# Optimization experiments

Hardware: AMD Instinct MI355X
Metric: run time of the kernel (lower is better)

Reference implementation:

```python
import jax, jax.numpy as jnp
import numpy as np

NEG_SLOPE = 0.2  # PyG GATConv default leaky_relu slope


def gat_layer(x, src, dst, W, a_src, a_dst, bias, heads, d, concat):
    # x: [N, in_dim]; src/dst: [E] (edges flow src -> dst, self-loops included)
    N = x.shape[0]
    h = (x @ W).reshape(N, heads, d)                      # [N, H, D]
    alpha_src = jnp.einsum('nhd,hd->nh', h, a_src)        # [N, H]
    alpha_dst = jnp.einsum('nhd,hd->nh', h, a_dst)        # [N, H]
    e = jax.nn.leaky_relu(alpha_src[src] + alpha_dst[dst], NEG_SLOPE)  # [E, H]
    # softmax over incoming edges of each destination node (segment softmax)
    m = jax.ops.segment_max(e, dst, num_segments=N)       # [N, H]
    ex = jnp.exp(e - m[dst])
    s = jax.ops.segment_sum(ex, dst, num_segments=N)      # [N, H]
    alpha = ex / s[dst]                                   # [E, H]
    msg = h[src] * alpha[..., None]                       # [E, H, D]
    out = jax.ops.segment_sum(msg, dst, num_segments=N)   # [N, H, D]
    out = out.reshape(N, heads * d) if concat else out.mean(axis=1)
    return out + bias


def setup_inputs() -> dict:
    key = jax.random.key(0)
    ks = jax.random.split(key, 12)
    N, E = 10000, 320000
    in_dim, hidden, heads, out_dim = 256, 64, 4, 40
    x = jax.random.normal(ks[0], (N, in_dim), dtype=jnp.float32)
    edge_index = jax.random.randint(ks[1], (2, E), 0, N, dtype=jnp.int64)
    s = 0.1
    return {
        'x': x,
        'edge_index': edge_index,
        'W1': jax.random.normal(ks[2], (in_dim, heads * hidden), jnp.float32) * s,
        'att_src1': jax.random.normal(ks[3], (heads, hidden), jnp.float32) * s,
        'att_dst1': jax.random.normal(ks[4], (heads, hidden), jnp.float32) * s,
        'bias1': jnp.zeros((heads * hidden,), jnp.float32),
        'W2': jax.random.normal(ks[5], (heads * hidden, out_dim), jnp.float32) * s,
        'att_src2': jax.random.normal(ks[6], (1, out_dim), jnp.float32) * s,
        'att_dst2': jax.random.normal(ks[7], (1, out_dim), jnp.float32) * s,
        'bias2': jnp.zeros((out_dim,), jnp.float32),
    }


def reference(x, edge_index, W1, att_src1, att_dst1, bias1, W2, att_src2, att_dst2, bias2):
    N = x.shape[0]
    # PyG GATConv adds self-loops by default
    loop = jnp.arange(N, dtype=edge_index.dtype)
    src = jnp.concatenate([edge_index[0], loop])
    dst = jnp.concatenate([edge_index[1], loop])
    h = gat_layer(x, src, dst, W1, att_src1, att_dst1, bias1, heads=4, d=64, concat=True)
    h = jax.nn.relu(h)
    out = gat_layer(h, src, dst, W2, att_src2, att_dst2, bias2, heads=1, d=40, concat=False)
    return jax.nn.log_softmax(out, axis=1)
```

## Files before the change

### kernel.cpp

```cpp
#include <hip/hip_runtime.h>
#include <hip/hip_bf16.h>
#include <math.h>

#define IN_DIM 256
#define C1 256
#define H1 4
#define OUT_DIM 40
#define W2PAD 48
#define NEG_SLOPE 0.2f
#define DSTRIDE 128

typedef __attribute__((ext_vector_type(8))) short bf16x8;
typedef __attribute__((ext_vector_type(4))) float f32x4;
typedef __attribute__((ext_vector_type(2))) float f32x2;

#define XS_LD 264

__device__ __forceinline__ unsigned short f2bf(float f) {
    union { float f; unsigned u; } c; c.f = f;
    unsigned r = c.u + 0x7fffu + ((c.u >> 16) & 1u);
    return (unsigned short)(r >> 16);
}

__device__ __forceinline__ unsigned char f2fp8(float f) {
    return (unsigned char)__builtin_amdgcn_cvt_pk_fp8_f32(f, 0.f, 0, false);
}

__device__ __forceinline__ float sel4(float4 v, int h) {
    float r = v.x;
    r = (h == 1) ? v.y : r;
    r = (h == 2) ? v.z : r;
    r = (h == 3) ? v.w : r;
    return r;
}

__device__ __forceinline__ float leaky(float v) {
    return (v >= 0.0f) ? v : NEG_SLOPE * v;
}

__global__ void k_prep(int* __restrict__ fill, const float* __restrict__ W1,
                       unsigned short* __restrict__ W1t, const float* __restrict__ W2,
                       unsigned short* __restrict__ W2t, const float* __restrict__ a_src2,
                       const float* __restrict__ a_dst2, float* __restrict__ w2s,
                       float* __restrict__ w2d, int N) {
    int t = threadIdx.x;
    int g = blockIdx.x * 256 + t;
    if (g < N) fill[g << 4] = 0;
    if (g < C1) {
        float s = 0.0f, d = 0.0f;
#pragma unroll
        for (int j = 0; j < OUT_DIM; ++j) {
            float w = W2[g * OUT_DIM + j];
            s += w * a_src2[j];
            d += w * a_dst2[j];
        }
        w2s[g] = s;
        w2d[g] = d;
    }
    if (g < W2PAD * C1) {
        int j = g >> 8, k = g & 255;
        W2t[g] = (j < OUT_DIM) ? f2bf(W2[k * OUT_DIM + j]) : 0;
    }
    __shared__ float s32[32][33];
    int b = blockIdx.x;
    int r0 = (b >> 3) * 32;
    int c0 = (b & 7) * 32;
    for (int i = t; i < 1024; i += 256) {
        int lr = i >> 5, lc = i & 31;
        s32[lr][lc] = W1[(r0 + lr) * 256 + c0 + lc];
    }
    __syncthreads();
    for (int i = t; i < 1024; i += 256) {
        int oc = i >> 5, ok = i & 31;
        W1t[(c0 + oc) * 256 + r0 + ok] = f2bf(s32[ok][oc]);
    }
}

__global__ void __launch_bounds__(256) k_fused1(
    const float* __restrict__ x, const unsigned short* __restrict__ W1t,
    const float* __restrict__ a_src, const float* __restrict__ a_dst,
    unsigned char* __restrict__ h1, float* __restrict__ as1, float* __restrict__ ad1,
    const int* __restrict__ ei, int* __restrict__ fill, unsigned short* __restrict__ srcs,
    int N, int E, int ET, int G1) {
    __shared__ unsigned short xs[64 * XS_LD];
    int t = threadIdx.x;

    if (blockIdx.x >= G1) {
        int eb = (blockIdx.x - G1) * 1024 + t;
#pragma unroll
        for (int k = 0; k < 4; ++k) {
            int e = eb + k * 256;
            if (e < ET) {
                int s, d;
                if (e < E) { s = ei[e]; d = ei[E + e]; }
                else       { s = e - E; d = s; }
                int pos = atomicAdd(&fill[d << 4], 1);
                srcs[(d << 7) + pos] = (unsigned short)s;
            }
        }
        return;
    }

    int n0 = blockIdx.x * 64;
    for (int i = t; i < 4096; i += 256) {
        int r = i >> 6, c4 = i & 63;
        int n = n0 + r;
        float4 v = (n < N) ? ((const float4*)x)[(size_t)n * 64 + c4]
                           : make_float4(0.f, 0.f, 0.f, 0.f);
        uint2 pk;
        pk.x = (unsigned)f2bf(v.x) | ((unsigned)f2bf(v.y) << 16);
        pk.y = (unsigned)f2bf(v.z) | ((unsigned)f2bf(v.w) << 16);
        *((uint2*)&xs[r * XS_LD + c4 * 4]) = pk;
    }
    __syncthreads();

    int wv = t >> 6, lane = t & 63;
    int quad = lane >> 4, ln = lane & 15;

    f32x4 acc[4][4];
#pragma unroll
    for (int mt = 0; mt < 4; ++mt)
#pragma unroll
        for (int nt = 0; nt < 4; ++nt) acc[mt][nt] = (f32x4){0.f, 0.f, 0.f, 0.f};

#pragma unroll
    for (int kb = 0; kb < 8; ++kb) {
        bf16x8 af[4], bf[4];
#pragma unroll
        for (int mt = 0; mt < 4; ++mt)
            af[mt] = *((bf16x8*)&xs[(mt * 16 + ln) * XS_LD + kb * 32 + quad * 8]);
#pragma unroll
        for (int nt = 0; nt < 4; ++nt)
            bf[nt] = *((const bf16x8*)(W1t + ((wv * 64 + nt * 16 + ln) * 256 + kb * 32 + quad * 8)));
#pragma unroll
        for (int mt = 0; mt < 4; ++mt)
#pragma unroll
            for (int nt = 0; nt < 4; ++nt)
                acc[mt][nt] = __builtin_amdgcn_mfma_f32_16x16x32_bf16(af[mt], bf[nt], acc[mt][nt], 0, 0, 0);
    }

    float asv[4], adv[4];
#pragma unroll
    for (int nt = 0; nt < 4; ++nt) {
        int col = wv * 64 + nt * 16 + ln;
        asv[nt] = a_src[col];
        adv[nt] = a_dst[col];
    }
#pragma unroll
    for (int mt = 0; mt < 4; ++mt) {
        float ds[4] = {0.f, 0.f, 0.f, 0.f};
        float dd[4] = {0.f, 0.f, 0.f, 0.f};
#pragma unroll
        for (int nt = 0; nt < 4; ++nt) {
#pragma unroll
            for (int r = 0; r < 4; ++r) {
                float v = acc[mt][nt][r];
                ds[r] += v * asv[nt];
                dd[r] += v * adv[nt];
            }
        }
#pragma unroll
        for (int r = 0; r < 4; ++r) {
            float vs = ds[r], vd = dd[r];
#pragma unroll
            for (int o = 1; o < 16; o <<= 1) {
                vs += __shfl_xor(vs, o);
                vd += __shfl_xor(vd, o);
            }
            if (ln == 0) {
                int node = n0 + mt * 16 + quad * 4 + r;
                if (node < N) {
                    as1[node * H1 + wv] = vs;
                    ad1[node * H1 + wv] = vd;
                }
            }
        }
    }

    __syncthreads();
    unsigned char* bt = (unsigned char*)xs;
#pragma unroll
    for (int mt = 0; mt < 4; ++mt)
#pragma unroll
        for (int nt = 0; nt < 4; ++nt)
#pragma unroll
            for (int r = 0; r < 4; ++r)
                bt[(mt * 16 + quad * 4 + r) * 256 + wv * 64 + nt * 16 + ln] = f2fp8(acc[mt][nt][r]);
    __syncthreads();
    const uint4* bt4 = (const uint4*)bt;
    uint4* h14 = (uint4*)(h1 + (size_t)n0 * C1);
    for (int i = t; i < 1024; i += 256) {
        int row = i >> 4;
        if (n0 + row < N) h14[i] = bt4[i];
    }
}

__global__ void __launch_bounds__(256) k_node1(
    const int* __restrict__ fill, const unsigned short* __restrict__ srcs,
    const float* __restrict__ as1f, const float* __restrict__ ad1f,
    const unsigned char* __restrict__ h1, const float* __restrict__ bias1,
    const float* __restrict__ w2s, const float* __restrict__ w2d,
    const unsigned short* __restrict__ W2t, unsigned short* __restrict__ h2b,
    float* __restrict__ as2, float* __restrict__ ad2, int N) {
    int w = threadIdx.x >> 6, lane = threadIdx.x & 63;
    int n = blockIdx.x * 4 + w;
    bool valid = (n < N);
    __shared__ float4 es[4][64];
    __shared__ unsigned short Abuf[16 * 256];
    int half = lane >> 5, hl = lane & 31;
    int h8 = hl >> 3;
    int start = n << 7;
    int end = start + (valid ? fill[n << 4] : 0);
    const float4* as4 = (const float4*)as1f;
    float4 adn = valid ? ((const float4*)ad1f)[n] : make_float4(0.f, 0.f, 0.f, 0.f);
    const float* esw = (const float*)&es[w][0];

    float4 S4 = make_float4(0.f, 0.f, 0.f, 0.f);
    float acc[8];
#pragma unroll
    for (int k = 0; k < 8; ++k) acc[k] = 0.f;

    for (int c = start; c < end; c += 64) {
        int cnt = min(64, end - c);
        int idx = c + lane;
        int sreg = (idx < end) ? (int)srcs[idx] : 0;
        float4 exv = make_float4(0.f, 0.f, 0.f, 0.f);
        if (idx < end) {
            float4 a = as4[sreg];
            exv.x = __expf(leaky(a.x + adn.x));
            exv.y = __expf(leaky(a.y + adn.y));
            exv.z = __expf(leaky(a.z + adn.z));
            exv.w = __expf(leaky(a.w + adn.w));
        }
        S4.x += exv.x; S4.y += exv.y; S4.z += exv.z; S4.w += exv.w;
        es[w][lane] = exv;

        int i = 0;
        for (; i + 7 < cnt; i += 8) {
            int s[4]; float a[4]; uint2 r[4];
#pragma unroll
            for (int k = 0; k < 4; ++k) {
                int j = i + 2 * k + half;
                s[k] = __shfl(sreg, j);
                a[k] = esw[j * 4 + h8];
            }
#pragma unroll
            for (int k = 0; k < 4; ++k)
                r[k] = *((const uint2*)(h1 + (size_t)s[k] * C1) + hl);
#pragma unroll
            for (int k = 0; k < 4; ++k) {
                f32x2 lo0 = __builtin_amdgcn_cvt_pk_f32_fp8(r[k].x, false);
                f32x2 hi0 = __builtin_amdgcn_cvt_pk_f32_fp8(r[k].x, true);
                f32x2 lo1 = __builtin_amdgcn_cvt_pk_f32_fp8(r[k].y, false);
                f32x2 hi1 = __builtin_amdgcn_cvt_pk_f32_fp8(r[k].y, true);
                acc[0] += a[k] * lo0.x; acc[1] += a[k] * lo0.y;
                acc[2] += a[k] * hi0.x; acc[3] += a[k] * hi0.y;
                acc[4] += a[k] * lo1.x; acc[5] += a[k] * lo1.y;
                acc[6] += a[k] * hi1.x; acc[7] += a[k] * hi1.y;
            }
        }
        for (; i < cnt; i += 2) {
            int j = i + half;
            int s0 = __shfl(sreg, j);
            float a0 = esw[j * 4 + h8];
            uint2 r0 = *((const uint2*)(h1 + (size_t)s0 * C1) + hl);
            f32x2 lo0 = __builtin_amdgcn_cvt_pk_f32_fp8(r0.x, false);
            f32x2 hi0 = __builtin_amdgcn_cvt_pk_f32_fp8(r0.x, true);
            f32x2 lo1 = __builtin_amdgcn_cvt_pk_f32_fp8(r0.y, false);
            f32x2 hi1 = __builtin_amdgcn_cvt_pk_f32_fp8(r0.y, true);
            acc[0] += a0 * lo0.x; acc[1] += a0 * lo0.y;
            acc[2] += a0 * hi0.x; acc[3] += a0 * hi0.y;
            acc[4] += a0 * lo1.x; acc[5] += a0 * lo1.y;
            acc[6] += a0 * hi1.x; acc[7] += a0 * hi1.y;
        }
    }

#pragma unroll
    for (int k = 0; k < 8; ++k) acc[k] += __shfl_xor(acc[k], 32);

#pragma unroll
    for (int o = 32; o > 0; o >>= 1) {
        S4.x += __shfl_xor(S4.x, o);
        S4.y += __shfl_xor(S4.y, o);
        S4.z += __shfl_xor(S4.z, o);
        S4.w += __shfl_xor(S4.w, o);
    }
    float iS = 1.0f / sel4(S4, h8);
    float4 b0 = ((const float4*)bias1)[hl * 2];
    float4 b1 = ((const float4*)bias1)[hl * 2 + 1];
    float v0 = fmaxf(acc[0] * iS + b0.x, 0.f);
    float v1 = fmaxf(acc[1] * iS + b0.y, 0.f);
    float v2 = fmaxf(acc[2] * iS + b0.z, 0.f);
    float v3 = fmaxf(acc[3] * iS + b0.w, 0.f);
    float v4 = fmaxf(acc[4] * iS + b1.x, 0.f);
    float v5 = fmaxf(acc[5] * iS + b1.y, 0.f);
    float v6 = fmaxf(acc[6] * iS + b1.z, 0.f);
    float v7 = fmaxf(acc[7] * iS + b1.w, 0.f);
    if (half == 0) {
        uint4 pk;
        pk.x = (unsigned)f2bf(v0) | ((unsigned)f2bf(v1) << 16);
        pk.y = (unsigned)f2bf(v2) | ((unsigned)f2bf(v3) << 16);
        pk.z = (unsigned)f2bf(v4) | ((unsigned)f2bf(v5) << 16);
        pk.w = (unsigned)f2bf(v6) | ((unsigned)f2bf(v7) << 16);
        ((uint4*)&Abuf[w * 256])[hl] = pk;
    }

    float4 ws0 = ((const float4*)w2s)[hl * 2];
    float4 ws1 = ((const float4*)w2s)[hl * 2 + 1];
    float4 wd0 = ((const float4*)w2d)[hl * 2];
    float4 wd1 = ((const float4*)w2d)[hl * 2 + 1];
    float ps = v0 * ws0.x + v1 * ws0.y + v2 * ws0.z + v3 * ws0.w
             + v4 * ws1.x + v5 * ws1.y + v6 * ws1.z + v7 * ws1.w;
    float pd = v0 * wd0.x + v1 * wd0.y + v2 * wd0.z + v3 * wd0.w
             + v4 * wd1.x + v5 * wd1.y + v6 * wd1.z + v7 * wd1.w;
#pragma unroll
    for (int o = 16; o > 0; o >>= 1) {
        ps += __shfl_xor(ps, o);
        pd += __shfl_xor(pd, o);
    }
    if (lane == 0 && valid) { as2[n] = ps; ad2[n] = pd; }

    __syncthreads();
    if (w < 3) {
        int quad = lane >> 4, ln = lane & 15;
        f32x4 accm = (f32x4){0.f, 0.f, 0.f, 0.f};
        const unsigned short* bbase = W2t + (w * 16 + ln) * 256;
#pragma unroll
        for (int kb = 0; kb < 8; ++kb) {
            bf16x8 af = *((bf16x8*)&Abuf[ln * 256 + kb * 32 + quad * 8]);
            bf16x8 bfr = *((const bf16x8*)(bbase + kb * 32 + quad * 8));
            accm = __builtin_amdgcn_mfma_f32_16x16x32_bf16(af, bfr, accm, 0, 0, 0);
        }
        int col = w * 16 + ln;
        if (col < OUT_DIM && quad == 0) {
#pragma unroll
            for (int r = 0; r < 4; ++r) {
                int node = blockIdx.x * 4 + r;
                if (node < N) h2b[(size_t)node * OUT_DIM + col] = f2bf(accm[r]);
            }
        }
    }
}

__global__ void __launch_bounds__(256) k_node2(
    const int* __restrict__ fill, const unsigned short* __restrict__ srcs,
    const float* __restrict__ as2, const float* __restrict__ ad2,
    const unsigned short* __restrict__ h2b, const float* __restrict__ bias2,
    float* __restrict__ out, int N) {
    int w = threadIdx.x >> 6, lane = threadIdx.x & 63;
    int n = blockIdx.x * 4 + w;
    if (n >= N) return;
    int g = lane / 10;
    int gl = lane - g * 10;
    int start = n << 7;
    int end = start + fill[n << 4];
    float adn = ad2[n];
    float S = 0.f;
    float acc0 = 0.f, acc1 = 0.f, acc2 = 0.f, acc3 = 0.f;

    for (int c = start; c < end; c += 64) {
        int cnt = min(64, end - c);
        int idx = c + lane;
        int sreg = (idx < end) ? (int)srcs[idx] : 0;
        float ex = (idx < end) ? __expf(leaky(as2[sreg] + adn)) : 0.f;
        S += ex;
        for (int i = 0; i < cnt; i += 12) {
            int j0 = i + g, j1 = i + 6 + g;
            int jc0 = min(j0, 63), jc1 = min(j1, 63);
            int su0 = __shfl(sreg, jc0), su1 = __shfl(sreg, jc1);
            float al0 = __shfl(ex, jc0), al1 = __shfl(ex, jc1);
            if (j0 >= cnt) al0 = 0.f;
            if (j1 >= cnt) al1 = 0.f;
            uint2 r0 = *((const uint2*)(h2b + (size_t)su0 * OUT_DIM) + gl);
            uint2 r1 = *((const uint2*)(h2b + (size_t)su1 * OUT_DIM) + gl);
            acc0 += al0 * __uint_as_float(r0.x << 16)         + al1 * __uint_as_float(r1.x << 16);
            acc1 += al0 * __uint_as_float(r0.x & 0xffff0000u) + al1 * __uint_as_float(r1.x & 0xffff0000u);
            acc2 += al0 * __uint_as_float(r0.y << 16)         + al1 * __uint_as_float(r1.y << 16);
            acc3 += al0 * __uint_as_float(r0.y & 0xffff0000u) + al1 * __uint_as_float(r1.y & 0xffff0000u);
        }
    }

    int l10 = min(lane + 10, 63), l20 = min(lane + 20, 63), l30 = min(lane + 30, 63);
    int l40 = min(lane + 40, 63), l50 = min(lane + 50, 63);
    float t0 = acc0 + __shfl(acc0, l10) + __shfl(acc0, l20) + __shfl(acc0, l30)
                    + __shfl(acc0, l40) + __shfl(acc0, l50);
    float t1 = acc1 + __shfl(acc1, l10) + __shfl(acc1, l20) + __shfl(acc1, l30)
                    + __shfl(acc1, l40) + __shfl(acc1, l50);
    float t2 = acc2 + __shfl(acc2, l10) + __shfl(acc2, l20) + __shfl(acc2, l30)
                    + __shfl(acc2, l40) + __shfl(acc2, l50);
    float t3 = acc3 + __shfl(acc3, l10) + __shfl(acc3, l20) + __shfl(acc3, l30)
                    + __shfl(acc3, l40) + __shfl(acc3, l50);
#pragma unroll
    for (int o = 32; o > 0; o >>= 1) S += __shfl_xor(S, o);

    bool act = lane < 10;
    float iS = 1.0f / S;
    float4 bz = make_float4(0.f, 0.f, 0.f, 0.f);
    if (act) bz = ((const float4*)bias2)[lane];
    float v0 = act ? (t0 * iS + bz.x) : -INFINITY;
    float v1 = act ? (t1 * iS + bz.y) : -INFINITY;
    float v2 = act ? (t2 * iS + bz.z) : -INFINITY;
    float v3 = act ? (t3 * iS + bz.w) : -INFINITY;
    float mx = fmaxf(fmaxf(v0, v1), fmaxf(v2, v3));
#pragma unroll
    for (int o = 8; o > 0; o >>= 1) mx = fmaxf(mx, __shfl_xor(mx, o));
    float e0 = act ? __expf(v0 - mx) : 0.f;
    float e1 = act ? __expf(v1 - mx) : 0.f;
    float e2 = act ? __expf(v2 - mx) : 0.f;
    float e3 = act ? __expf(v3 - mx) : 0.f;
    float esum = (e0 + e1) + (e2 + e3);
#pragma unroll
    for (int o = 8; o > 0; o >>= 1) esum += __shfl_xor(esum, o);
    if (act) {
        float l = mx + logf(esum);
        *((float4*)(out + (size_t)n * OUT_DIM) + lane) = make_float4(v0 - l, v1 - l, v2 - l, v3 - l);
    }
}

extern "C" void kernel_launch(void* const* d_in, const int* in_sizes, int n_in,
                              void* d_out, int out_size, void* d_ws, size_t ws_size,
                              hipStream_t stream) {
    const float* x        = (const float*)d_in[0];
    const int*   ei       = (const int*)d_in[1];
    const float* W1       = (const float*)d_in[2];
    const float* att_src1 = (const float*)d_in[3];
    const float* att_dst1 = (const float*)d_in[4];
    const float* bias1    = (const float*)d_in[5];
    const float* W2       = (const float*)d_in[6];
    const float* att_src2 = (const float*)d_in[7];
    const float* att_dst2 = (const float*)d_in[8];
    const float* bias2    = (const float*)d_in[9];
    float* out = (float*)d_out;

    const int N  = in_sizes[0] / IN_DIM;
    const int E  = in_sizes[1] / 2;
    const int ET = E + N;

    char* base = (char*)d_ws;
    auto alloc = [&](size_t bytes) {
        char* p = base;
        base += (bytes + 255) & ~(size_t)255;
        return p;
    };
    unsigned char*  h1    = (unsigned char*)alloc((size_t)N * C1);
    unsigned short* W1t   = (unsigned short*)alloc((size_t)C1 * C1 * 2);
    unsigned short* W2t   = (unsigned short*)alloc((size_t)W2PAD * C1 * 2);
    unsigned short* h2b   = (unsigned short*)alloc((size_t)N * OUT_DIM * 2);
    float* as1   = (float*)alloc((size_t)N * H1 * 4);
    float* ad1   = (float*)alloc((size_t)N * H1 * 4);
    float* as2   = (float*)alloc((size_t)N * 4);
    float* ad2   = (float*)alloc((size_t)N * 4);
    float* w2s   = (float*)alloc((size_t)C1 * 4);
    float* w2d   = (float*)alloc((size_t)C1 * 4);
    int* fill    = (int*)alloc((size_t)N * 16 * 4);
    unsigned short* srcs = (unsigned short*)alloc((size_t)N * DSTRIDE * 2);

    const int G1 = (N + 63) / 64;
    const int GS = (ET + 1023) / 1024;

    k_prep<<<64, 256, 0, stream>>>(fill, W1, W1t, W2, W2t, att_src2, att_dst2, w2s, w2d, N);
    k_fused1<<<G1 + GS, 256, 0, stream>>>(x, W1t, att_src1, att_dst1, h1, as1, ad1,
                                          ei, fill, srcs, N, E, ET, G1);
    k_node1<<<(N + 3) / 4, 256, 0, stream>>>(fill, srcs, as1, ad1, h1, bias1, w2s, w2d,
                                             W2t, h2b, as2, ad2, N);
    k_node2<<<(N + 3) / 4, 256, 0, stream>>>(fill, srcs, as2, ad2, h2b, bias2, out, N);
}
```

Before: 138.9 us.

## Fuse all GAT stages into one cooperative persistent kernel with grid syncs

Replaces the four separate launches (prep, fused GEMM/scatter, node1, node2) with a single cooperative kernel of 1024 blocks that runs each stage in turn, separated by grid.sync(). Node loops become grid-stride over fixed persistent blocks. The goal is to remove per-launch overhead and inter-kernel gaps. In exchange, the GEMM phase now gets only 1024-G1 blocks for the edge scatter, grid syncs add their own cost, and occupancy is limited by the cooperative launch. The old kernels stay as a fallback if the cooperative launch fails.

New measurement: 535.3 us. 286% more time.

```diff
diff --git a/kernel.cpp b/kernel.cpp
--- a/kernel.cpp
+++ b/kernel.cpp
@@ -1,6 +1,9 @@
 #include <hip/hip_runtime.h>
+#include <hip/hip_cooperative_groups.h>
 #include <hip/hip_bf16.h>
 #include <math.h>
+
+namespace cg = cooperative_groups;
 
 #define IN_DIM 256
 #define C1 256
@@ -9,6 +12,7 @@
 #define W2PAD 48
 #define NEG_SLOPE 0.2f
 #define DSTRIDE 128
+#define GRID_NB 1024
 
 typedef __attribute__((ext_vector_type(8))) short bf16x8;
 typedef __attribute__((ext_vector_type(4))) float f32x4;
@@ -36,6 +40,385 @@
 
 __device__ __forceinline__ float leaky(float v) {
     return (v >= 0.0f) ? v : NEG_SLOPE * v;
+}
+
+__global__ void __launch_bounds__(256, 4) k_gat(
+    const float* __restrict__ x, const int* __restrict__ ei,
+    const float* __restrict__ W1, const float* __restrict__ a_src1,
+    const float* __restrict__ a_dst1, const float* __restrict__ bias1,
+    const float* __restrict__ W2, const float* __restrict__ a_src2,
+    const float* __restrict__ a_dst2, const float* __restrict__ bias2,
+    float* __restrict__ out,
+    unsigned char* h1, unsigned short* W1t, unsigned short* W2t,
+    unsigned short* h2b, float* as1, float* ad1, float* as2, float* ad2,
+    float* w2s, float* w2d, int* fill, unsigned short* srcs,
+    int N, int E, int ET, int G1) {
+    cg::grid_group grid = cg::this_grid();
+    __shared__ __align__(16) char smem[64 * XS_LD * 2];
+    const int t = threadIdx.x;
+    const int b = blockIdx.x;
+    const int nb = GRID_NB;
+
+    if (b < 64) {
+        int g = b * 256 + t;
+        if (g < N) fill[g << 4] = 0;
+        if (g < C1) {
+            float s = 0.0f, d = 0.0f;
+#pragma unroll
+            for (int j = 0; j < OUT_DIM; ++j) {
+                float w = W2[g * OUT_DIM + j];
+                s += w * a_src2[j];
+                d += w * a_dst2[j];
+            }
+            w2s[g] = s;
+            w2d[g] = d;
+        }
+        if (g < W2PAD * C1) {
+            int j = g >> 8, k = g & 255;
+            W2t[g] = (j < OUT_DIM) ? f2bf(W2[k * OUT_DIM + j]) : 0;
+        }
+        float (*s32)[33] = (float (*)[33])smem;
+        int r0 = (b >> 3) * 32;
+        int c0 = (b & 7) * 32;
+        for (int i = t; i < 1024; i += 256) {
+            int lr = i >> 5, lc = i & 31;
+            s32[lr][lc] = W1[(r0 + lr) * 256 + c0 + lc];
+        }
+        __syncthreads();
+        for (int i = t; i < 1024; i += 256) {
+            int oc = i >> 5, ok = i & 31;
+            W1t[(c0 + oc) * 256 + r0 + ok] = f2bf(s32[ok][oc]);
+        }
+    }
+    grid.sync();
+
+    if (b >= G1) {
+        int sb = b - G1, nsb = nb - G1;
+        for (int e = sb * 256 + t; e < ET; e += nsb * 256) {
+            int s, d;
+            if (e < E) { s = ei[e]; d = ei[E + e]; }
+            else       { s = e - E; d = s; }
+            int pos = atomicAdd(&fill[d << 4], 1);
+            srcs[(d << 7) + pos] = (unsigned short)s;
+        }
+    } else {
+        unsigned short* xs = (unsigned short*)smem;
+        int n0 = b * 64;
+        for (int i = t; i < 4096; i += 256) {
+            int r = i >> 6, c4 = i & 63;
+            int n = n0 + r;
+            float4 v = (n < N) ? ((const float4*)x)[(size_t)n * 64 + c4]
+                               : make_float4(0.f, 0.f, 0.f, 0.f);
+            uint2 pk;
+            pk.x = (unsigned)f2bf(v.x) | ((unsigned)f2bf(v.y) << 16);
+            pk.y = (unsigned)f2bf(v.z) | ((unsigned)f2bf(v.w) << 16);
+            *((uint2*)&xs[r * XS_LD + c4 * 4]) = pk;
+        }
+        __syncthreads();
+
+        int wv = t >> 6, lane = t & 63;
+        int quad = lane >> 4, ln = lane & 15;
+
+        f32x4 acc[4][4];
+#pragma unroll
+        for (int mt = 0; mt < 4; ++mt)
+#pragma unroll
+            for (int nt = 0; nt < 4; ++nt) acc[mt][nt] = (f32x4){0.f, 0.f, 0.f, 0.f};
+
+#pragma unroll
+        for (int kb = 0; kb < 8; ++kb) {
+            bf16x8 af[4], bfv[4];
+#pragma unroll
+            for (int mt = 0; mt < 4; ++mt)
+                af[mt] = *((bf16x8*)&xs[(mt * 16 + ln) * XS_LD + kb * 32 + quad * 8]);
+#pragma unroll
+            for (int nt = 0; nt < 4; ++nt)
+                bfv[nt] = *((const bf16x8*)(W1t + ((wv * 64 + nt * 16 + ln) * 256 + kb * 32 + quad * 8)));
+#pragma unroll
+            for (int mt = 0; mt < 4; ++mt)
+#pragma unroll
+                for (int nt = 0; nt < 4; ++nt)
+                    acc[mt][nt] = __builtin_amdgcn_mfma_f32_16x16x32_bf16(af[mt], bfv[nt], acc[mt][nt], 0, 0, 0);
+        }
+
+        float asv[4], adv[4];
+#pragma unroll
+        for (int nt = 0; nt < 4; ++nt) {
+            int col = wv * 64 + nt * 16 + ln;
+            asv[nt] = a_src1[col];
+            adv[nt] = a_dst1[col];
+        }
+#pragma unroll
+        for (int mt = 0; mt < 4; ++mt) {
+            float ds[4] = {0.f, 0.f, 0.f, 0.f};
+            float dd[4] = {0.f, 0.f, 0.f, 0.f};
+#pragma unroll
+            for (int nt = 0; nt < 4; ++nt) {
+#pragma unroll
+                for (int r = 0; r < 4; ++r) {
+                    float v = acc[mt][nt][r];
+                    ds[r] += v * asv[nt];
+                    dd[r] += v * adv[nt];
+                }
+            }
+#pragma unroll
+            for (int r = 0; r < 4; ++r) {
+                float vs = ds[r], vd = dd[r];
+#pragma unroll
+                for (int o = 1; o < 16; o <<= 1) {
+                    vs += __shfl_xor(vs, o);
+                    vd += __shfl_xor(vd, o);
+                }
+                if (ln == 0) {
+                    int node = n0 + mt * 16 + quad * 4 + r;
+                    if (node < N) {
+                        as1[node * H1 + wv] = vs;
+                        ad1[node * H1 + wv] = vd;
+                    }
+                }
+            }
+        }
+
+        __syncthreads();
+        unsigned char* bt = (unsigned char*)xs;
+#pragma unroll
+        for (int mt = 0; mt < 4; ++mt)
+#pragma unroll
+            for (int nt = 0; nt < 4; ++nt)
+#pragma unroll
+                for (int r = 0; r < 4; ++r)
+                    bt[(mt * 16 + quad * 4 + r) * 256 + wv * 64 + nt * 16 + ln] = f2fp8(acc[mt][nt][r]);
+        __syncthreads();
+        const uint4* bt4 = (const uint4*)bt;
+        uint4* h14 = (uint4*)(h1 + (size_t)n0 * C1);
+        for (int i = t; i < 1024; i += 256) {
+            int row = i >> 4;
+            if (n0 + row < N) h14[i] = bt4[i];
+        }
+    }
+    grid.sync();
+
+    {
+        const int w = t >> 6, lane = t & 63;
+        const int half = lane >> 5, hl = lane & 31;
+        const int h8 = hl >> 3;
+        float4* esb = (float4*)smem;
+        unsigned short* Abuf = (unsigned short*)(smem + 4096);
+        const float* esw = (const float*)(esb + w * 64);
+        const float4* as4 = (const float4*)as1;
+        const int NG = (N + 3) >> 2;
+
+        for (int ub = b; ub < NG; ub += nb) {
+            int n = ub * 4 + w;
+            bool valid = (n < N);
+            int start = n << 7;
+            int end = start + (valid ? fill[n << 4] : 0);
+            float4 adn = valid ? ((const float4*)ad1)[n] : make_float4(0.f, 0.f, 0.f, 0.f);
+
+            float4 S4 = make_float4(0.f, 0.f, 0.f, 0.f);
+            float acc[8];
+#pragma unroll
+            for (int k = 0; k < 8; ++k) acc[k] = 0.f;
+
+            for (int c = start; c < end; c += 64) {
+                int cnt = min(64, end - c);
+                int idx = c + lane;
+                int sreg = (idx < end) ? (int)srcs[idx] : 0;
+                float4 exv = make_float4(0.f, 0.f, 0.f, 0.f);
+                if (idx < end) {
+                    float4 a = as4[sreg];
+                    exv.x = __expf(leaky(a.x + adn.x));
+                    exv.y = __expf(leaky(a.y + adn.y));
+                    exv.z = __expf(leaky(a.z + adn.z));
+                    exv.w = __expf(leaky(a.w + adn.w));
+                }
+                S4.x += exv.x; S4.y += exv.y; S4.z += exv.z; S4.w += exv.w;
+                esb[w * 64 + lane] = exv;
+
+                int i = 0;
+                for (; i + 7 < cnt; i += 8) {
+                    int s[4]; float a[4]; uint2 r[4];
+#pragma unroll
+                    for (int k = 0; k < 4; ++k) {
+                        int j = i + 2 * k + half;
+                        s[k] = __shfl(sreg, j);
+                        a[k] = esw[j * 4 + h8];
+                    }
+#pragma unroll
+                    for (int k = 0; k < 4; ++k)
+                        r[k] = *((const uint2*)(h1 + (size_t)s[k] * C1) + hl);
+#pragma unroll
+                    for (int k = 0; k < 4; ++k) {
+                        f32x2 lo0 = __builtin_amdgcn_cvt_pk_f32_fp8(r[k].x, false);
+                        f32x2 hi0 = __builtin_amdgcn_cvt_pk_f32_fp8(r[k].x, true);
+                        f32x2 lo1 = __builtin_amdgcn_cvt_pk_f32_fp8(r[k].y, false);
+                        f32x2 hi1 = __builtin_amdgcn_cvt_pk_f32_fp8(r[k].y, true);
+                        acc[0] += a[k] * lo0.x; acc[1] += a[k] * lo0.y;
+                        acc[2] += a[k] * hi0.x; acc[3] += a[k] * hi0.y;
+                        acc[4] += a[k] * lo1.x; acc[5] += a[k] * lo1.y;
+                        acc[6] += a[k] * hi1.x; acc[7] += a[k] * hi1.y;
+                    }
+                }
+                for (; i < cnt; i += 2) {
+                    int j = i + half;
+                    int s0 = __shfl(sreg, j);
+                    float a0 = esw[j * 4 + h8];
+                    uint2 r0 = *((const uint2*)(h1 + (size_t)s0 * C1) + hl);
+                    f32x2 lo0 = __builtin_amdgcn_cvt_pk_f32_fp8(r0.x, false);
+                    f32x2 hi0 = __builtin_amdgcn_cvt_pk_f32_fp8(r0.x, true);
+                    f32x2 lo1 = __builtin_amdgcn_cvt_pk_f32_fp8(r0.y, false);
+                    f32x2 hi1 = __builtin_amdgcn_cvt_pk_f32_fp8(r0.y, true);
+                    acc[0] += a0 * lo0.x; acc[1] += a0 * lo0.y;
+                    acc[2] += a0 * hi0.x; acc[3] += a0 * hi0.y;
+                    acc[4] += a0 * lo1.x; acc[5] += a0 * lo1.y;
+                    acc[6] += a0 * hi1.x; acc[7] += a0 * hi1.y;
+                }
+            }
+
+#pragma unroll
+            for (int k = 0; k < 8; ++k) acc[k] += __shfl_xor(acc[k], 32);
+
+#pragma unroll
+            for (int o = 32; o > 0; o >>= 1) {
+                S4.x += __shfl_xor(S4.x, o);
+                S4.y += __shfl_xor(S4.y, o);
+                S4.z += __shfl_xor(S4.z, o);
+                S4.w += __shfl_xor(S4.w, o);
+            }
+            float iS = 1.0f / sel4(S4, h8);
+            float4 b0 = ((const float4*)bias1)[hl * 2];
+            float4 b1 = ((const float4*)bias1)[hl * 2 + 1];
+            float v0 = fmaxf(acc[0] * iS + b0.x, 0.f);
+            float v1 = fmaxf(acc[1] * iS + b0.y, 0.f);
+            float v2 = fmaxf(acc[2] * iS + b0.z, 0.f);
+            float v3 = fmaxf(acc[3] * iS + b0.w, 0.f);
+            float v4 = fmaxf(acc[4] * iS + b1.x, 0.f);
+            float v5 = fmaxf(acc[5] * iS + b1.y, 0.f);
+            float v6 = fmaxf(acc[6] * iS + b1.z, 0.f);
+            float v7 = fmaxf(acc[7] * iS + b1.w, 0.f);
+            if (half == 0) {
+                uint4 pk;
+                pk.x = (unsigned)f2bf(v0) | ((unsigned)f2bf(v1) << 16);
+                pk.y = (unsigned)f2bf(v2) | ((unsigned)f2bf(v3) << 16);
+                pk.z = (unsigned)f2bf(v4) | ((unsigned)f2bf(v5) << 16);
+                pk.w = (unsigned)f2bf(v6) | ((unsigned)f2bf(v7) << 16);
+                ((uint4*)&Abuf[w * 256])[hl] = pk;
+            }
+
+            float4 ws0 = ((const float4*)w2s)[hl * 2];
+            float4 ws1 = ((const float4*)w2s)[hl * 2 + 1];
+            float4 wd0 = ((const float4*)w2d)[hl * 2];
+            float4 wd1 = ((const float4*)w2d)[hl * 2 + 1];
+            float ps = v0 * ws0.x + v1 * ws0.y + v2 * ws0.z + v3 * ws0.w
+                     + v4 * ws1.x + v5 * ws1.y + v6 * ws1.z + v7 * ws1.w;
+            float pd = v0 * wd0.x + v1 * wd0.y + v2 * wd0.z + v3 * wd0.w
+                     + v4 * wd1.x + v5 * wd1.y + v6 * wd1.z + v7 * wd1.w;
+#pragma unroll
+            for (int o = 16; o > 0; o >>= 1) {
+                ps += __shfl_xor(ps, o);
+                pd += __shfl_xor(pd, o);
+            }
+            if (lane == 0 && valid) { as2[n] = ps; ad2[n] = pd; }
+
+            __syncthreads();
+            if (w < 3) {
+                int quad = lane >> 4, ln = lane & 15;
+                f32x4 accm = (f32x4){0.f, 0.f, 0.f, 0.f};
+                const unsigned short* bbase = W2t + (w * 16 + ln) * 256;
+#pragma unroll
+                for (int kb = 0; kb < 8; ++kb) {
+                    bf16x8 af = *((bf16x8*)&Abuf[ln * 256 + kb * 32 + quad * 8]);
+                    bf16x8 bfr = *((const bf16x8*)(bbase + kb * 32 + quad * 8));
+                    accm = __builtin_amdgcn_mfma_f32_16x16x32_bf16(af, bfr, accm, 0, 0, 0);
+                }
+                int col = w * 16 + ln;
+                if (col < OUT_DIM && quad == 0) {
+#pragma unroll
+                    for (int r = 0; r < 4; ++r) {
+                        int node = ub * 4 + r;
+                        if (node < N) h2b[(size_t)node * OUT_DIM + col] = f2bf(accm[r]);
+                    }
+                }
+            }
+            __syncthreads();
+        }
+    }
+    grid.sync();
+
+    {
+        const int w = t >> 6, lane = t & 63;
+        const int g = lane / 10;
+        const int gl = lane - g * 10;
+        const int NG = (N + 3) >> 2;
+
+        for (int ub = b; ub < NG; ub += nb) {
+            int n = ub * 4 + w;
+            if (n >= N) continue;
+            int start = n << 7;
+            int end = start + fill[n << 4];
+            float adn = ad2[n];
+            float S = 0.f;
+            float acc0 = 0.f, acc1 = 0.f, acc2 = 0.f, acc3 = 0.f;
+
+            for (int c = start; c < end; c += 64) {
+                int cnt = min(64, end - c);
+                int idx = c + lane;
+                int sreg = (idx < end) ? (int)srcs[idx] : 0;
+                float ex = (idx < end) ? __expf(leaky(as2[sreg] + adn)) : 0.f;
+                S += ex;
+                for (int i = 0; i < cnt; i += 12) {
+                    int j0 = i + g, j1 = i + 6 + g;
+                    int jc0 = min(j0, 63), jc1 = min(j1, 63);
+                    int su0 = __shfl(sreg, jc0), su1 = __shfl(sreg, jc1);
+                    float al0 = __shfl(ex, jc0), al1 = __shfl(ex, jc1);
+                    if (j0 >= cnt) al0 = 0.f;
+                    if (j1 >= cnt) al1 = 0.f;
+                    uint2 r0 = *((const uint2*)(h2b + (size_t)su0 * OUT_DIM) + gl);
+                    uint2 r1 = *((const uint2*)(h2b + (size_t)su1 * OUT_DIM) + gl);
+                    acc0 += al0 * __uint_as_float(r0.x << 16)         + al1 * __uint_as_float(r1.x << 16);
+                    acc1 += al0 * __uint_as_float(r0.x & 0xffff0000u) + al1 * __uint_as_float(r1.x & 0xffff0000u);
+                    acc2 += al0 * __uint_as_float(r0.y << 16)         + al1 * __uint_as_float(r1.y << 16);
+                    acc3 += al0 * __uint_as_float(r0.y & 0xffff0000u) + al1 * __uint_as_float(r1.y & 0xffff0000u);
+                }
+            }
+
+            int l10 = min(lane + 10, 63), l20 = min(lane + 20, 63), l30 = min(lane + 30, 63);
+            int l40 = min(lane + 40, 63), l50 = min(lane + 50, 63);
+            float t0 = acc0 + __shfl(acc0, l10) + __shfl(acc0, l20) + __shfl(acc0, l30)
+                            + __shfl(acc0, l40) + __shfl(acc0, l50);
+            float t1 = acc1 + __shfl(acc1, l10) + __shfl(acc1, l20) + __shfl(acc1, l30)
+                            + __shfl(acc1, l40) + __shfl(acc1, l50);
+            float t2 = acc2 + __shfl(acc2, l10) + __shfl(acc2, l20) + __shfl(acc2, l30)
+                            + __shfl(acc2, l40) + __shfl(acc2, l50);
+            float t3 = acc3 + __shfl(acc3, l10) + __shfl(acc3, l20) + __shfl(acc3, l30)
+                            + __shfl(acc3, l40) + __shfl(acc3, l50);
+#pragma unroll
+            for (int o = 32; o > 0; o >>= 1) S += __shfl_xor(S, o);
+
+            bool act = lane < 10;
+            float iS = 1.0f / S;
+            float4 bz = make_float4(0.f, 0.f, 0.f, 0.f);
+            if (act) bz = ((const float4*)bias2)[lane];
+            float v0 = act ? (t0 * iS + bz.x) : -INFINITY;
+            float v1 = act ? (t1 * iS + bz.y) : -INFINITY;
+            float v2 = act ? (t2 * iS + bz.z) : -INFINITY;
+            float v3 = act ? (t3 * iS + bz.w) : -INFINITY;
+            float mx = fmaxf(fmaxf(v0, v1), fmaxf(v2, v3));
+#pragma unroll
+            for (int o = 8; o > 0; o >>= 1) mx = fmaxf(mx, __shfl_xor(mx, o));
+            float e0 = act ? __expf(v0 - mx) : 0.f;
+            float e1 = act ? __expf(v1 - mx) : 0.f;
+            float e2 = act ? __expf(v2 - mx) : 0.f;
+            float e3 = act ? __expf(v3 - mx) : 0.f;
+            float esum = (e0 + e1) + (e2 + e3);
+#pragma unroll
+            for (int o = 8; o > 0; o >>= 1) esum += __shfl_xor(esum, o);
+            if (act) {
+                float l = mx + logf(esum);
+                *((float4*)(out + (size_t)n * OUT_DIM) + lane) = make_float4(v0 - l, v1 - l, v2 - l, v3 - l);
+            }
+        }
+    }
 }
 
 __global__ void k_prep(int* __restrict__ fill, const float* __restrict__ W1,
@@ -125,18 +508,18 @@
 
 #pragma unroll
     for (int kb = 0; kb < 8; ++kb) {
-        bf16x8 af[4], bf[4];
+        bf16x8 af[4], bfv[4];
 #pragma unroll
         for (int mt = 0; mt < 4; ++mt)
             af[mt] = *((bf16x8*)&xs[(mt * 16 + ln) * XS_LD + kb * 32 + quad * 8]);
 #pragma unroll
         for (int nt = 0; nt < 4; ++nt)
-            bf[nt] = *((const bf16x8*)(W1t + ((wv * 64 + nt * 16 + ln) * 256 + kb * 32 + quad * 8)));
+            bfv[nt] = *((const bf16x8*)(W1t + ((wv * 64 + nt * 16 + ln) * 256 + kb * 32 + quad * 8)));
 #pragma unroll
         for (int mt = 0; mt < 4; ++mt)
 #pragma unroll
             for (int nt = 0; nt < 4; ++nt)
-                acc[mt][nt] = __builtin_amdgcn_mfma_f32_16x16x32_bf16(af[mt], bf[nt], acc[mt][nt], 0, 0, 0);
+                acc[mt][nt] = __builtin_amdgcn_mfma_f32_16x16x32_bf16(af[mt], bfv[nt], acc[mt][nt], 0, 0, 0);
     }
 
     float asv[4], adv[4];
@@ -456,12 +839,25 @@
     unsigned short* srcs = (unsigned short*)alloc((size_t)N * DSTRIDE * 2);
 
     const int G1 = (N + 63) / 64;
-    const int GS = (ET + 1023) / 1024;
-
-    k_prep<<<64, 256, 0, stream>>>(fill, W1, W1t, W2, W2t, att_src2, att_dst2, w2s, w2d, N);
-    k_fused1<<<G1 + GS, 256, 0, stream>>>(x, W1t, att_src1, att_dst1, h1, as1, ad1,
-                                          ei, fill, srcs, N, E, ET, G1);
-    k_node1<<<(N + 3) / 4, 256, 0, stream>>>(fill, srcs, as1, ad1, h1, bias1, w2s, w2d,
-                                             W2t, h2b, as2, ad2, N);
-    k_node2<<<(N + 3) / 4, 256, 0, stream>>>(fill, srcs, as2, ad2, h2b, bias2, out, N);
-}
+
+    int Ni = N, Ei = E, ETi = ET, G1i = G1;
+    void* args[] = { (void*)&x, (void*)&ei, (void*)&W1, (void*)&att_src1, (void*)&att_dst1,
+                     (void*)&bias1, (void*)&W2, (void*)&att_src2, (void*)&att_dst2,
+                     (void*)&bias2, (void*)&out,
+                     (void*)&h1, (void*)&W1t, (void*)&W2t, (void*)&h2b,
+                     (void*)&as1, (void*)&ad1, (void*)&as2, (void*)&ad2,
+                     (void*)&w2s, (void*)&w2d, (void*)&fill, (void*)&srcs,
+                     (void*)&Ni, (void*)&Ei, (void*)&ETi, (void*)&G1i };
+
+    hipError_t err = hipLaunchCooperativeKernel((void*)k_gat, dim3(GRID_NB), dim3(256),
+                                                args, 0, stream);
+    if (err != hipSuccess) {
+        const int GS = (ET + 1023) / 1024;
+        k_prep<<<64, 256, 0, stream>>>(fill, W1, W1t, W2, W2t, att_src2, att_dst2, w2s, w2d, N);
+        k_fused1<<<G1 + GS, 256, 0, stream>>>(x, W1t, att_src1, att_dst1, h1, as1, ad1,
+                                              ei, fill, srcs, N, E, ET, G1);
+        k_node1<<<(N + 3) / 4, 256, 0, stream>>>(fill, srcs, as1, ad1, h1, bias1, w2s, w2d,
+                                                 W2t, h2b, as2, ad2, N);
+        k_node2<<<(N + 3) / 4, 256, 0, stream>>>(fill, srcs, as2, ad2, h2b, bias2, out, N);
+    }
+}
```
